# Kernel tuning notes

Measured on AMD Instinct MI355X. Metric: run time of the kernel, lower is better.

Reference implementation:

```python
import jax, jax.numpy as jnp
import numpy as np

EMBED = 2048
N_EXPERTS = 64
TOP_K = 8


def setup_inputs() -> dict:
    key = jax.random.key(0)
    k_x, k_w, k_b = jax.random.split(key, 3)
    inputs = jax.random.normal(k_x, (8, 4096, EMBED), dtype=jnp.float32)
    # nn.Linear(embed_size, num_experts): weight [E, D], bias [E]
    bound = 1.0 / np.sqrt(EMBED)
    W = jax.random.uniform(k_w, (N_EXPERTS, EMBED), dtype=jnp.float32, minval=-bound, maxval=bound)
    b = jax.random.uniform(k_b, (N_EXPERTS,), dtype=jnp.float32, minval=-bound, maxval=bound)
    return {"inputs": inputs, "W": W, "b": b}


def reference(inputs, W, b):
    # scores: [B, S, E]
    scores = jnp.einsum("bsd,ed->bse", inputs, W) + b
    topk_scores, indices = jax.lax.top_k(scores, TOP_K)  # [B,S,K]
    # scatter topk_scores into a zero mask (non-selected slots stay 0.0)
    onehot = jax.nn.one_hot(indices, N_EXPERTS, dtype=scores.dtype)  # [B,S,K,E]
    mask = jnp.einsum("bske,bsk->bse", onehot, topk_scores)
    router_output = jax.nn.softmax(mask, axis=-1)
    return (router_output, indices)
```

## Files before the change

### kernel.cpp

```cpp
#include <hip/hip_runtime.h>
#include <math.h>

#define N_TOKENS 32768
#define EMBED    2048
#define NEXP     64
#define TOPK     8
#define BM       64
#define BK       64
#define NCH      (EMBED / BK)
#define SCS      65
#define THRESH   1e-4f
#define WELEMS   (NEXP * EMBED)
#define FIXGRID  1024

typedef __attribute__((ext_vector_type(8)))  short short8;
typedef __attribute__((ext_vector_type(4)))  short short4v;
typedef __attribute__((ext_vector_type(16))) float f32x16;

__device__ __forceinline__ unsigned short bf16rne(float f) {
  unsigned int fb = __float_as_uint(f);
  return (unsigned short)((fb + 0x7FFFu + ((fb >> 16) & 1u)) >> 16);
}

__device__ __forceinline__ void cvt4(float4 f, short4v* h, short4v* l) {
  float fs[4] = {f.x, f.y, f.z, f.w};
  short4v hh, ll;
#pragma unroll
  for (int i = 0; i < 4; ++i) {
    unsigned short hr = bf16rne(fs[i]);
    hh[i] = (short)hr;
    float hf = __uint_as_float((unsigned int)hr << 16);
    ll[i] = (short)bf16rne(fs[i] - hf);
  }
  *h = hh; *l = ll;
}

__global__ void split_w(const float* __restrict__ W, short* __restrict__ wh,
                        short* __restrict__ wl) {
  const int T = blockIdx.x * 256 + threadIdx.x;
  const int n = T >> 8, kg8 = T & 255;
  const float4* W4 = (const float4*)W;
  float4 a = W4[n * 512 + kg8 * 2];
  float4 b = W4[n * 512 + kg8 * 2 + 1];
  short4v h0, l0, h1, l1;
  cvt4(a, &h0, &l0); cvt4(b, &h1, &l1);
  short* dh = &wh[(kg8 * 64 + n) * 8];
  short* dl = &wl[(kg8 * 64 + n) * 8];
  *(short4v*)dh = h0; *(short4v*)(dh + 4) = h1;
  *(short4v*)dl = l0; *(short4v*)(dl + 4) = l1;
}

__global__ __launch_bounds__(256, 4)
void router_kernel(const float* __restrict__ x, const short* __restrict__ wh,
                   const short* __restrict__ wl, const float* __restrict__ bias,
                   int* __restrict__ gcnt, int* __restrict__ glist,
                   float* __restrict__ out) {
  __shared__ float4 lx[2][1024];
  float* sc = (float*)&lx[0][0];

  const int tid  = threadIdx.x;
  const int t0   = blockIdx.x * BM;
  const int lane = tid & 63;
  const int w    = tid >> 6;
  const int half = lane >> 5;
  const int r5   = lane & 31;
  const int tw   = (w & 1) * 32;
  const int ew   = (w >> 1) * 32;

  const float4* x4g = (const float4*)x;
  const short8* Bh  = (const short8*)wh;
  const short8* Bl  = (const short8*)wl;
  const int boff = half * 64 + ew + r5;

  const int row16 = tid >> 4;
  const int s4    = tid & 15;
  const int c4sw  = s4 ^ row16;
  const int wbase = (tid & 192);

  f32x16 acc;
#pragma unroll
  for (int i = 0; i < 16; ++i) acc[i] = 0.f;

#pragma unroll
  for (int i = 0; i < 4; ++i) {
    const float4* gp = x4g + (size_t)(t0 + row16 + 16 * i) * (EMBED / 4) + c4sw;
    __builtin_amdgcn_global_load_lds((const void*)gp, (void*)&lx[0][i * 256 + wbase],
                                     16, 0, 0);
  }

  const int arow  = tw + r5;
  const int am    = arow & 15;
  const int abase = (arow >> 4) * 256 + am * 16;

  for (int ch = 0; ch < NCH; ++ch) {
    const int buf = ch & 1;
    __syncthreads();

    if (ch + 1 < NCH) {
#pragma unroll
      for (int i = 0; i < 4; ++i) {
        const float4* gp = x4g + (size_t)(t0 + row16 + 16 * i) * (EMBED / 4)
                               + (ch + 1) * 16 + c4sw;
        __builtin_amdgcn_global_load_lds((const void*)gp,
                                         (void*)&lx[buf ^ 1][i * 256 + wbase], 16, 0, 0);
      }
    }

    short8 bh[4], bl[4];
#pragma unroll
    for (int s = 0; s < 4; ++s) {
      const int bi = (ch * 4 + s) * 128 + boff;
      bh[s] = Bh[bi]; bl[s] = Bl[bi];
    }

#pragma unroll
    for (int s = 0; s < 4; ++s) {
      const int c0 = s * 4 + half * 2;
      float4 fa = lx[buf][abase + (c0 ^ am)];
      float4 fb = lx[buf][abase + ((c0 + 1) ^ am)];
      short4v h0, l0, h1, l1;
      cvt4(fa, &h0, &l0); cvt4(fb, &h1, &l1);
      short8 ah, al;
#pragma unroll
      for (int j = 0; j < 4; ++j) { ah[j] = h0[j]; ah[j + 4] = h1[j];
                                    al[j] = l0[j]; al[j + 4] = l1[j]; }
      acc = __builtin_amdgcn_mfma_f32_32x32x16_bf16(ah, bh[s], acc, 0, 0, 0);
      acc = __builtin_amdgcn_mfma_f32_32x32x16_bf16(ah, bl[s], acc, 0, 0, 0);
      acc = __builtin_amdgcn_mfma_f32_32x32x16_bf16(al, bh[s], acc, 0, 0, 0);
    }
  }

  __syncthreads();

#pragma unroll
  for (int reg = 0; reg < 16; ++reg) {
    const int row = (reg & 3) + 8 * (reg >> 2) + 4 * half;
    sc[(tw + row) * SCS + ew + r5] = acc[reg];
  }
  __syncthreads();

  float* rout = out;
  float* iout = out + (size_t)N_TOKENS * NEXP;
  const float bias_l = bias[lane];

  for (int tb = 0; tb < 4; ++tb) {
    const int tbase = w * 16 + tb * 4;
    float orig[4]; unsigned cur[4];
#pragma unroll
    for (int i = 0; i < 4; ++i) {
      orig[i] = sc[(tbase + i) * SCS + lane] + bias_l;
      unsigned b = __float_as_uint(orig[i]);
      unsigned u = b ^ (((unsigned)((int)b >> 31)) | 0x80000000u);
      cur[i] = (u & 0xFFFFFFC0u) | (63u - (unsigned)lane);
    }
    float m[4], Z[4], ming[4], prev[4], morig[4];
    int myidx[4]; bool sel[4];
#pragma unroll
    for (int i = 0; i < 4; ++i) { sel[i] = false; morig[i] = 0.f; myidx[i] = 0; ming[i] = 1e30f; }

#pragma unroll
    for (int r = 0; r < 9; ++r) {
      unsigned v[4];
#pragma unroll
      for (int i = 0; i < 4; ++i) v[i] = cur[i];
#pragma unroll
      for (int s2 = 1; s2 < 64; s2 <<= 1) {
#pragma unroll
        for (int i = 0; i < 4; ++i) {
          unsigned o = (unsigned)__shfl_xor((int)v[i], s2);
          v[i] = v[i] > o ? v[i] : o;
        }
      }
#pragma unroll
      for (int i = 0; i < 4; ++i) {
        unsigned vb = (v[i] & 0x80000000u) ? (v[i] ^ 0x80000000u) : ~v[i];
        float fv = __uint_as_float(vb);
        if (r == 0) { m[i] = fmaxf(fv, 0.f); Z[i] = 56.f * expf(-m[i]) + expf(fv - m[i]); }
        else {
          ming[i] = fminf(ming[i], prev[i] - fv);
          if (r < 8) Z[i] += expf(fv - m[i]);
        }
        prev[i] = fv;
        if (r < 8) {
          if (lane == r) myidx[i] = 63 - (int)(v[i] & 63u);
          if (cur[i] == v[i]) { sel[i] = true; morig[i] = orig[i]; cur[i] = 0u; }
        }
      }
    }
#pragma unroll
    for (int i = 0; i < 4; ++i) {
      const int t = tbase + i;
      if (ming[i] < THRESH) {
        if (lane == 0) { int p = atomicAdd(gcnt, 1); glist[p] = t0 + t; }
      } else {
        const float p = expf(morig[i] - m[i]) / Z[i];
        rout[(size_t)(t0 + t) * NEXP + lane] = p;
        if (lane < TOPK) iout[(size_t)(t0 + t) * TOPK + lane] = (float)myidx[i];
      }
    }
  }
}

__global__ __launch_bounds__(256, 4)
void fixup_kernel(const float* __restrict__ x, const float* __restrict__ Wf,
                  const float* __restrict__ bias, const int* __restrict__ gcnt,
                  const int* __restrict__ glist, float* __restrict__ out) {
  __shared__ float4 xsh[512];
  __shared__ double sco[NEXP];
  const int tid  = threadIdx.x;
  const int lane = tid & 63;
  const int w    = tid >> 6;
  float* rout = out;
  float* iout = out + (size_t)N_TOKENS * NEXP;
  const int cnt = *gcnt;

  for (int j = blockIdx.x; j < cnt; j += FIXGRID) {
    const int tok = glist[j];
    const float4* xr = (const float4*)x + (size_t)tok * 512;
    xsh[tid] = xr[tid];
    xsh[tid + 256] = xr[tid + 256];
    __syncthreads();

    for (int i = 0; i < 16; ++i) {
      const int e = w * 16 + i;
      const float4* wr = (const float4*)Wf + (size_t)e * 512;
      double a = 0.0;
#pragma unroll
      for (int q = 0; q < 8; ++q) {
        float4 wv = wr[q * 64 + lane];
        float4 xv = xsh[q * 64 + lane];
        a = fma((double)xv.x, (double)wv.x, a);
        a = fma((double)xv.y, (double)wv.y, a);
        a = fma((double)xv.z, (double)wv.z, a);
        a = fma((double)xv.w, (double)wv.w, a);
      }
#pragma unroll
      for (int s2 = 1; s2 < 64; s2 <<= 1) a += __shfl_xor(a, s2);
      if (lane == 0) sco[e] = a + (double)bias[e];
    }
    __syncthreads();

    if (w == 0) {
      const double orig = sco[lane];
      double curd = orig, vals[8];
      int myidx = 0; double mym = 0.0;
#pragma unroll
      for (int r = 0; r < 8; ++r) {
        double v = curd; int id = lane;
#pragma unroll
        for (int s2 = 1; s2 < 64; s2 <<= 1) {
          const double ov = __shfl_xor(v, s2);
          const int    oi = __shfl_xor(id, s2);
          if (ov > v || (ov == v && oi < id)) { v = ov; id = oi; }
        }
        vals[r] = v;
        if (lane == r)  myidx = id;
        if (lane == id) { mym = orig; curd = -1e300; }
      }
      const double md = fmax(vals[0], 0.0);
      double Zd = 56.0 * exp(-md);
#pragma unroll
      for (int r = 0; r < 8; ++r) Zd += exp(vals[r] - md);
      const double p = exp(mym - md) / Zd;
      rout[(size_t)tok * NEXP + lane] = (float)p;
      if (lane < TOPK) iout[(size_t)tok * TOPK + lane] = (float)myidx;
    }
    __syncthreads();
  }
}

extern "C" void kernel_launch(void* const* d_in, const int* in_sizes, int n_in,
                              void* d_out, int out_size, void* d_ws, size_t ws_size,
                              hipStream_t stream) {
  const float* x = (const float*)d_in[0];
  const float* W = (const float*)d_in[1];
  const float* b = (const float*)d_in[2];
  short* wh = (short*)d_ws;
  short* wl = wh + WELEMS;
  int* gcnt  = (int*)(wl + WELEMS);
  int* glist = gcnt + 4;

  hipMemsetAsync(gcnt, 0, 16, stream);
  split_w<<<64, 256, 0, stream>>>(W, wh, wl);
  router_kernel<<<N_TOKENS / BM, 256, 0, stream>>>(x, wh, wl, b, gcnt, glist,
                                                   (float*)d_out);
  fixup_kernel<<<FIXGRID, 256, 0, stream>>>(x, W, b, gcnt, glist, (float*)d_out);
}
```

Before: 469.9 us.

## Triple-buffer x tiles with vmcnt waits and use hardware bf16 pack conversion

The x staging goes from two LDS buffers to three, prefetching two chunks ahead. A single barrier per chunk now follows an explicit vmcnt wait instead of a full syncthreads before each issue. The software bf16 round-to-nearest split is replaced with v_cvt_pk_bf16_f32 packed conversions, which cuts ALU work in the inner loop. The counter memset is folded into split_w to drop a launch, and launch_bounds drops to 2 waves per SIMD to allow for the larger LDS footprint. This risks lower occupancy, and the hand-written vmcnt counts must match the outstanding loads exactly.

```diff
diff --git a/kernel.cpp b/kernel.cpp
--- a/kernel.cpp
+++ b/kernel.cpp
@@ -14,48 +14,52 @@
 #define FIXGRID  1024
 
 typedef __attribute__((ext_vector_type(8)))  short short8;
-typedef __attribute__((ext_vector_type(4)))  short short4v;
 typedef __attribute__((ext_vector_type(16))) float f32x16;
-
-__device__ __forceinline__ unsigned short bf16rne(float f) {
-  unsigned int fb = __float_as_uint(f);
-  return (unsigned short)((fb + 0x7FFFu + ((fb >> 16) & 1u)) >> 16);
-}
-
-__device__ __forceinline__ void cvt4(float4 f, short4v* h, short4v* l) {
-  float fs[4] = {f.x, f.y, f.z, f.w};
-  short4v hh, ll;
-#pragma unroll
-  for (int i = 0; i < 4; ++i) {
-    unsigned short hr = bf16rne(fs[i]);
-    hh[i] = (short)hr;
-    float hf = __uint_as_float((unsigned int)hr << 16);
-    ll[i] = (short)bf16rne(fs[i] - hf);
-  }
-  *h = hh; *l = ll;
+typedef __attribute__((ext_vector_type(4)))  unsigned int uint4v;
+
+__device__ __forceinline__ unsigned pkbf(float a, float b) {
+  unsigned r;
+  asm("v_cvt_pk_bf16_f32 %0, %1, %2" : "=v"(r) : "v"(a), "v"(b));
+  return r;
+}
+
+__device__ __forceinline__ void cvt8(float4 fa, float4 fb, short8* h8, short8* l8) {
+  const unsigned h0 = pkbf(fa.x, fa.y), h1 = pkbf(fa.z, fa.w);
+  const unsigned h2 = pkbf(fb.x, fb.y), h3 = pkbf(fb.z, fb.w);
+  const float l0 = fa.x - __uint_as_float(h0 << 16);
+  const float l1 = fa.y - __uint_as_float(h0 & 0xFFFF0000u);
+  const float l2 = fa.z - __uint_as_float(h1 << 16);
+  const float l3 = fa.w - __uint_as_float(h1 & 0xFFFF0000u);
+  const float l4 = fb.x - __uint_as_float(h2 << 16);
+  const float l5 = fb.y - __uint_as_float(h2 & 0xFFFF0000u);
+  const float l6 = fb.z - __uint_as_float(h3 << 16);
+  const float l7 = fb.w - __uint_as_float(h3 & 0xFFFF0000u);
+  const uint4v H = {h0, h1, h2, h3};
+  const uint4v L = {pkbf(l0, l1), pkbf(l2, l3), pkbf(l4, l5), pkbf(l6, l7)};
+  *h8 = __builtin_bit_cast(short8, H);
+  *l8 = __builtin_bit_cast(short8, L);
 }
 
 __global__ void split_w(const float* __restrict__ W, short* __restrict__ wh,
-                        short* __restrict__ wl) {
+                        short* __restrict__ wl, int* __restrict__ gcnt) {
+  if (blockIdx.x == 0 && threadIdx.x == 0) *gcnt = 0;
   const int T = blockIdx.x * 256 + threadIdx.x;
   const int n = T >> 8, kg8 = T & 255;
   const float4* W4 = (const float4*)W;
   float4 a = W4[n * 512 + kg8 * 2];
   float4 b = W4[n * 512 + kg8 * 2 + 1];
-  short4v h0, l0, h1, l1;
-  cvt4(a, &h0, &l0); cvt4(b, &h1, &l1);
-  short* dh = &wh[(kg8 * 64 + n) * 8];
-  short* dl = &wl[(kg8 * 64 + n) * 8];
-  *(short4v*)dh = h0; *(short4v*)(dh + 4) = h1;
-  *(short4v*)dl = l0; *(short4v*)(dl + 4) = l1;
-}
-
-__global__ __launch_bounds__(256, 4)
+  short8 h, l;
+  cvt8(a, b, &h, &l);
+  *(short8*)&wh[(kg8 * 64 + n) * 8] = h;
+  *(short8*)&wl[(kg8 * 64 + n) * 8] = l;
+}
+
+__global__ __launch_bounds__(256, 2)
 void router_kernel(const float* __restrict__ x, const short* __restrict__ wh,
                    const short* __restrict__ wl, const float* __restrict__ bias,
                    int* __restrict__ gcnt, int* __restrict__ glist,
                    float* __restrict__ out) {
-  __shared__ float4 lx[2][1024];
+  __shared__ float4 lx[3][1024];
   float* sc = (float*)&lx[0][0];
 
   const int tid  = threadIdx.x;
@@ -77,34 +81,31 @@
   const int c4sw  = s4 ^ row16;
   const int wbase = (tid & 192);
 
-  f32x16 acc;
-#pragma unroll
-  for (int i = 0; i < 16; ++i) acc[i] = 0.f;
-
-#pragma unroll
-  for (int i = 0; i < 4; ++i) {
-    const float4* gp = x4g + (size_t)(t0 + row16 + 16 * i) * (EMBED / 4) + c4sw;
-    __builtin_amdgcn_global_load_lds((const void*)gp, (void*)&lx[0][i * 256 + wbase],
-                                     16, 0, 0);
-  }
+  const float4* gbase = x4g + (size_t)(t0 + row16) * (EMBED / 4) + c4sw;
+
+#pragma unroll
+  for (int i = 0; i < 4; ++i)
+    __builtin_amdgcn_global_load_lds((const void*)(gbase + (size_t)16 * i * (EMBED / 4)),
+                                     (void*)&lx[0][i * 256 + wbase], 16, 0, 0);
+#pragma unroll
+  for (int i = 0; i < 4; ++i)
+    __builtin_amdgcn_global_load_lds((const void*)(gbase + (size_t)16 * i * (EMBED / 4) + 16),
+                                     (void*)&lx[1][i * 256 + wbase], 16, 0, 0);
 
   const int arow  = tw + r5;
   const int am    = arow & 15;
   const int abase = (arow >> 4) * 256 + am * 16;
 
+  f32x16 acc;
+#pragma unroll
+  for (int i = 0; i < 16; ++i) acc[i] = 0.f;
+
+  int bc = 0, bp = 2;
   for (int ch = 0; ch < NCH; ++ch) {
-    const int buf = ch & 1;
-    __syncthreads();
-
-    if (ch + 1 < NCH) {
-#pragma unroll
-      for (int i = 0; i < 4; ++i) {
-        const float4* gp = x4g + (size_t)(t0 + row16 + 16 * i) * (EMBED / 4)
-                               + (ch + 1) * 16 + c4sw;
-        __builtin_amdgcn_global_load_lds((const void*)gp,
-                                         (void*)&lx[buf ^ 1][i * 256 + wbase], 16, 0, 0);
-      }
-    }
+    if (ch + 1 < NCH) asm volatile("s_waitcnt vmcnt(4)" ::: "memory");
+    else              asm volatile("s_waitcnt vmcnt(0)" ::: "memory");
+    __builtin_amdgcn_s_barrier();
+    __builtin_amdgcn_sched_barrier(0);
 
     short8 bh[4], bl[4];
 #pragma unroll
@@ -112,22 +113,29 @@
       const int bi = (ch * 4 + s) * 128 + boff;
       bh[s] = Bh[bi]; bl[s] = Bl[bi];
     }
+    __builtin_amdgcn_sched_barrier(0);
+
+    if (ch + 2 < NCH) {
+#pragma unroll
+      for (int i = 0; i < 4; ++i)
+        __builtin_amdgcn_global_load_lds(
+            (const void*)(gbase + (size_t)16 * i * (EMBED / 4) + (ch + 2) * 16),
+            (void*)&lx[bp][i * 256 + wbase], 16, 0, 0);
+    }
 
 #pragma unroll
     for (int s = 0; s < 4; ++s) {
       const int c0 = s * 4 + half * 2;
-      float4 fa = lx[buf][abase + (c0 ^ am)];
-      float4 fb = lx[buf][abase + ((c0 + 1) ^ am)];
-      short4v h0, l0, h1, l1;
-      cvt4(fa, &h0, &l0); cvt4(fb, &h1, &l1);
+      float4 fa = lx[bc][abase + (c0 ^ am)];
+      float4 fb = lx[bc][abase + ((c0 + 1) ^ am)];
       short8 ah, al;
-#pragma unroll
-      for (int j = 0; j < 4; ++j) { ah[j] = h0[j]; ah[j + 4] = h1[j];
-                                    al[j] = l0[j]; al[j + 4] = l1[j]; }
+      cvt8(fa, fb, &ah, &al);
       acc = __builtin_amdgcn_mfma_f32_32x32x16_bf16(ah, bh[s], acc, 0, 0, 0);
       acc = __builtin_amdgcn_mfma_f32_32x32x16_bf16(ah, bl[s], acc, 0, 0, 0);
       acc = __builtin_amdgcn_mfma_f32_32x32x16_bf16(al, bh[s], acc, 0, 0, 0);
     }
+    bc = (bc == 2) ? 0 : bc + 1;
+    bp = (bp == 2) ? 0 : bp + 1;
   }
 
   __syncthreads();
@@ -280,8 +288,7 @@
   int* gcnt  = (int*)(wl + WELEMS);
   int* glist = gcnt + 4;
 
-  hipMemsetAsync(gcnt, 0, 16, stream);
-  split_w<<<64, 256, 0, stream>>>(W, wh, wl);
+  split_w<<<64, 256, 0, stream>>>(W, wh, wl, gcnt);
   router_kernel<<<N_TOKENS / BM, 256, 0, stream>>>(x, wh, wl, b, gcnt, glist,
                                                    (float*)d_out);
   fixup_kernel<<<FIXGRID, 256, 0, stream>>>(x, W, b, gcnt, glist, (float*)d_out);
```

New measurement: 465.9 us. Within noise of the previous version (-0.9%).
